# Optimization experiments

Measured on AMD Instinct MI355X. Metric: run time of the kernel, lower is better.

The kernel has to match this reference:

```python
import jax, jax.numpy as jnp
import numpy as np

EPS = 1e-5

def _lin(x, w, b):
    return x @ w + b

def _ln(x, scale, bias):
    m = jnp.mean(x, axis=-1, keepdims=True)
    v = jnp.var(x, axis=-1, keepdims=True)
    return (x - m) / jnp.sqrt(v + EPS) * scale + bias

def setup_inputs() -> dict:
    key = jax.random.key(0)
    B, N, F, OUT, TRI = 4, 128, 128, 128, 8
    ks = iter(jax.random.split(key, 64))
    def lin_params(fan_in, fan_out):
        s = 1.0 / np.sqrt(fan_in)
        w = jax.random.uniform(next(ks), (fan_in, fan_out), minval=-s, maxval=s, dtype=jnp.float32)
        b = jax.random.uniform(next(ks), (fan_out,), minval=-s, maxval=s, dtype=jnp.float32)
        return w, b
    inp = {}
    inp['node_fts'] = jax.random.normal(next(ks), (B, N, F), dtype=jnp.float32)
    inp['edge_fts'] = jax.random.normal(next(ks), (B, N, N, F), dtype=jnp.float32)
    inp['graph_fts'] = jax.random.normal(next(ks), (B, F), dtype=jnp.float32)
    inp['hidden'] = jax.random.normal(next(ks), (B, N, F), dtype=jnp.float32)
    inp['adj_matrix'] = jax.random.randint(next(ks), (B, N, N), 0, 2, dtype=jnp.int32)
    inp['m1_w'], inp['m1_b'] = lin_params(2 * F, OUT)
    inp['m2_w'], inp['m2_b'] = lin_params(2 * F, OUT)
    inp['me_w'], inp['me_b'] = lin_params(F, OUT)
    inp['mg_w'], inp['mg_b'] = lin_params(F, OUT)
    inp['mlp1_w'], inp['mlp1_b'] = lin_params(OUT, OUT)
    inp['mlp2_w'], inp['mlp2_b'] = lin_params(OUT, OUT)
    inp['o1_w'], inp['o1_b'] = lin_params(2 * F, OUT)
    inp['o2_w'], inp['o2_b'] = lin_params(OUT, OUT)
    inp['t1_w'], inp['t1_b'] = lin_params(2 * F, TRI)
    inp['t2_w'], inp['t2_b'] = lin_params(2 * F, TRI)
    inp['te1_w'], inp['te1_b'] = lin_params(F, TRI)
    inp['te2_w'], inp['te2_b'] = lin_params(F, TRI)
    inp['te3_w'], inp['te3_b'] = lin_params(F, TRI)
    inp['tg_w'], inp['tg_b'] = lin_params(F, TRI)
    inp['o3_w'], inp['o3_b'] = lin_params(TRI, OUT)
    inp['norm_scale'] = jnp.ones((OUT,), dtype=jnp.float32)
    inp['norm_bias'] = jnp.zeros((OUT,), dtype=jnp.float32)
    return inp

def reference(node_fts, edge_fts, graph_fts, hidden, adj_matrix,
              m1_w, m1_b, m2_w, m2_b, me_w, me_b, mg_w, mg_b,
              mlp1_w, mlp1_b, mlp2_w, mlp2_b,
              o1_w, o1_b, o2_w, o2_b,
              t1_w, t1_b, t2_w, t2_b,
              te1_w, te1_b, te2_w, te2_b, te3_w, te3_b,
              tg_w, tg_b, o3_w, o3_b, norm_scale, norm_bias):
    z = jnp.concatenate([node_fts, hidden], axis=-1)          # [B,N,2F]
    msg_1 = _lin(z, m1_w, m1_b)                                # [B,N,H]
    msg_2 = _lin(z, m2_w, m2_b)
    msg_e = _lin(edge_fts, me_w, me_b)                         # [B,N,N,H]
    msg_g = _lin(graph_fts, mg_w, mg_b)                        # [B,H]
    msgs = msg_1[:, None, :, :] + msg_2[:, :, None, :] + msg_e + msg_g[:, None, None, :]
    # msg_mlp: ReLU -> Linear -> ReLU -> Linear
    msgs = _lin(jax.nn.relu(_lin(jax.nn.relu(msgs), mlp1_w, mlp1_b)), mlp2_w, mlp2_b)
    # triplet messages (note: original code reuses t_1 for tri_3 -- faithful)
    tri_1 = _lin(z, t1_w, t1_b)                                # [B,N,T]
    tri_2 = _lin(z, t2_w, t2_b)
    tri_3 = _lin(z, t1_w, t1_b)
    tri_e_1 = _lin(edge_fts, te1_w, te1_b)                     # [B,N,N,T]
    tri_e_2 = _lin(edge_fts, te2_w, te2_b)
    tri_e_3 = _lin(edge_fts, te3_w, te3_b)
    tri_g = _lin(graph_fts, tg_w, tg_b)                        # [B,T]
    triplets = (tri_1[:, :, None, None, :] + tri_2[:, None, :, None, :]
                + tri_3[:, None, None, :, :]
                + tri_e_1[:, :, :, None, :] + tri_e_2[:, :, None, :, :]
                + tri_e_3[:, None, :, :, :]
                + tri_g[:, None, None, None, :])               # [B,N,N,N,T]
    tri_msgs = _lin(jnp.max(triplets, axis=1), o3_w, o3_b)     # [B,N,N,OUT]
    tri_msgs = _ln(jax.nn.relu(tri_msgs), norm_scale, norm_bias)
    # masked max aggregation
    maxarg = jnp.where(adj_matrix[..., None] == 1, msgs, -1e9)
    msgs_agg = jnp.max(maxarg, axis=1)                         # [B,N,H]
    out = jax.nn.relu(_lin(z, o1_w, o1_b) + _lin(msgs_agg, o2_w, o2_b))
    out = _ln(out, norm_scale, norm_bias)
    return out, tri_msgs
```

## Files before the change

kernel.cpp:

```cpp
#include <hip/hip_runtime.h>
#include <hip/hip_bf16.h>
#include <cstddef>
#include <cstdint>
#include <cstring>

typedef __attribute__((ext_vector_type(8))) short bf16x8;
typedef __attribute__((ext_vector_type(4))) float f32x4;
typedef unsigned short ushort_t;

__device__ __forceinline__ ushort_t f2b(float f) {
    uint32_t x = __float_as_uint(f);
    uint32_t r = (x + 0x7FFFu + ((x >> 16) & 1u)) >> 16;
    return (ushort_t)r;
}
__device__ __forceinline__ float b2f(ushort_t u) {
    return __uint_as_float(((uint32_t)u) << 16);
}
__device__ __forceinline__ uint32_t pk2(float x, float y) {
    __hip_bfloat162 h = __float22bfloat162_rn(float2{x, y});
    uint32_t u;
    __builtin_memcpy(&u, &h, 4);
    return u;
}

__global__ void prep_kernel(const float* __restrict__ m1_w, const float* __restrict__ m2_w,
                            const float* __restrict__ o1_w, const float* __restrict__ t1_w,
                            const float* __restrict__ t2_w,
                            const float* __restrict__ me_w, const float* __restrict__ mlp1_w,
                            const float* __restrict__ mlp2_w,
                            const float* __restrict__ te1_w, const float* __restrict__ te2_w,
                            const float* __restrict__ te3_w,
                            const float* __restrict__ graph_fts,
                            const float* __restrict__ mg_w, const float* __restrict__ mg_b,
                            const float* __restrict__ m1_b,
                            const float* __restrict__ tg_w, const float* __restrict__ t2_b,
                            const float* __restrict__ tg_b,
                            ushort_t* __restrict__ Wnt,
                            ushort_t* __restrict__ Wme, ushort_t* __restrict__ Wm1,
                            ushort_t* __restrict__ Wm2, ushort_t* __restrict__ TEt,
                            float* __restrict__ G1, float* __restrict__ TG) {
    int idx = blockIdx.x * 256 + threadIdx.x;
    if (idx < 106496) {
        int o = idx >> 8, k = idx & 255;
        float v = 0.0f;
        if (o < 128)       v = m1_w[k * 128 + o];
        else if (o < 256)  v = m2_w[k * 128 + (o - 128)];
        else if (o < 384)  v = o1_w[k * 128 + (o - 256)];
        else if (o < 392)  v = t1_w[k * 8 + (o - 384)];
        else if (o < 400)  v = t2_w[k * 8 + (o - 392)];
        Wnt[idx] = f2b(v);
    } else if (idx < 122880) {
        int t = idx - 106496, o = t >> 7, h = t & 127;
        Wme[t] = f2b(me_w[h * 128 + o]);
    } else if (idx < 139264) {
        int t = idx - 122880, o = t >> 7, h = t & 127;
        Wm1[t] = f2b(mlp1_w[h * 128 + o]);
    } else if (idx < 155648) {
        int t = idx - 139264, o = t >> 7, h = t & 127;
        Wm2[t] = f2b(mlp2_w[h * 128 + o]);
    } else if (idx < 159744) {
        int t = idx - 155648, c = t >> 7, h = t & 127;
        float v = 0.0f;
        if (c < 8)       v = te1_w[h * 8 + c];
        else if (c < 16) v = te2_w[h * 8 + (c - 8)];
        else if (c < 24) v = te3_w[h * 8 + (c - 16)];
        TEt[t] = f2b(v);
    } else if (idx < 160256) {
        int t = idx - 159744, b = t >> 7, h = t & 127;
        float a = m1_b[h] + mg_b[h];
        #pragma unroll 4
        for (int k = 0; k < 128; k++) a = fmaf(graph_fts[b * 128 + k], mg_w[k * 128 + h], a);
        G1[t] = a;
    } else if (idx < 160288) {
        int t = idx - 160256, b = t >> 3, tt = t & 7;
        float a = t2_b[tt] + tg_b[tt];
        #pragma unroll 4
        for (int k = 0; k < 128; k++) a = fmaf(graph_fts[b * 128 + k], tg_w[k * 8 + tt], a);
        TG[t] = a;
    }
}

__global__ __launch_bounds__(256)
void node_gemm(const float* __restrict__ node_fts, const float* __restrict__ hidden,
               const ushort_t* __restrict__ Wnt,
               const float* __restrict__ G1, const float* __restrict__ m2_b,
               const float* __restrict__ o1_b, const float* __restrict__ t1_b,
               const float* __restrict__ TG,
               float* __restrict__ M1, float* __restrict__ M2, float* __restrict__ O1z,
               float* __restrict__ T1v, float* __restrict__ TT2) {
    __shared__ ushort_t Zs[32 * 256];
    char* Zb = (char*)Zs;
    const int tid = threadIdx.x;
    const int blk = blockIdx.x;
    const int rowblk = blk >> 1, colh = blk & 1;
    const int b = rowblk >> 2, q = rowblk & 3;
    const int row0 = b * 128 + q * 32;
    const int w = tid >> 6, l = tid & 63, g = l >> 4, lq = l & 15;

    const float4* nsrc = reinterpret_cast<const float4*>(node_fts + (size_t)row0 * 128);
    const float4* hsrc = reinterpret_cast<const float4*>(hidden + (size_t)row0 * 128);
    #pragma unroll
    for (int p = 0; p < 8; p++) {
        int idx = tid + p * 256;
        int r = idx >> 6, c4 = idx & 63;
        float4 v = (c4 < 32) ? nsrc[r * 32 + c4] : hsrc[r * 32 + (c4 - 32)];
        uint2 pk;
        pk.x = pk2(v.x, v.y);
        pk.y = pk2(v.z, v.w);
        *reinterpret_cast<uint2*>(Zb + r * 512 + (((c4 >> 1) ^ (r & 7)) << 4) + (c4 & 1) * 8) = pk;
    }
    __syncthreads();

    for (int mt = colh * 13 + w; mt < colh * 13 + 13; mt += 4) {
        f32x4 acc0 = (f32x4){0.f, 0.f, 0.f, 0.f};
        f32x4 acc1 = (f32x4){0.f, 0.f, 0.f, 0.f};
        const ushort_t* arow = Wnt + (size_t)(mt * 16 + lq) * 256;
        #pragma unroll
        for (int ks = 0; ks < 8; ks++) {
            bf16x8 a = *reinterpret_cast<const bf16x8*>(arow + ks * 32 + g * 8);
            int j0 = lq, j1 = 16 + lq;
            bf16x8 b0 = *reinterpret_cast<const bf16x8*>(Zb + j0 * 512 + (((ks * 4 + g) ^ (j0 & 7)) << 4));
            bf16x8 b1 = *reinterpret_cast<const bf16x8*>(Zb + j1 * 512 + (((ks * 4 + g) ^ (j1 & 7)) << 4));
            acc0 = __builtin_amdgcn_mfma_f32_16x16x32_bf16(a, b0, acc0, 0, 0, 0);
            acc1 = __builtin_amdgcn_mfma_f32_16x16x32_bf16(a, b1, acc1, 0, 0, 0);
        }
        #pragma unroll
        for (int half = 0; half < 2; half++) {
            const f32x4 acc = half ? acc1 : acc0;
            const int grow = row0 + half * 16 + lq;
            #pragma unroll
            for (int c = 0; c < 4; c++) {
                int o = mt * 16 + g * 4 + c;
                float v = acc[c];
                if (o < 128)       M1[(size_t)grow * 128 + o] = v + G1[b * 128 + o];
                else if (o < 256)  M2[(size_t)grow * 128 + (o - 128)] = v + m2_b[o - 128];
                else if (o < 384)  O1z[(size_t)grow * 128 + (o - 256)] = v + o1_b[o - 256];
                else if (o < 392)  T1v[(size_t)grow * 8 + (o - 384)] = v + t1_b[o - 384];
                else if (o < 400)  TT2[(size_t)grow * 8 + (o - 392)] = v + TG[b * 8 + (o - 392)];
            }
        }
    }
}

__device__ __forceinline__ void mmv(const ushort_t* __restrict__ Wt, const char* Xa,
                                    f32x4 acc[2][4], int o_blk, int j_blk, int g, int lq) {
    #pragma unroll
    for (int ks = 0; ks < 4; ks++) {
        bf16x8 a[2], bb[4];
        #pragma unroll
        for (int m = 0; m < 2; m++)
            a[m] = *reinterpret_cast<const bf16x8*>(Wt + (size_t)(o_blk + m * 16 + lq) * 128 + ks * 32 + g * 8);
        #pragma unroll
        for (int n = 0; n < 4; n++) {
            int j = j_blk + n * 16 + lq;
            bb[n] = *reinterpret_cast<const bf16x8*>(Xa + j * 256 + (((ks * 4 + g) ^ (j & 7)) << 4));
        }
        #pragma unroll
        for (int m = 0; m < 2; m++)
            #pragma unroll
            for (int n = 0; n < 4; n++)
                acc[m][n] = __builtin_amdgcn_mfma_f32_16x16x32_bf16(a[m], bb[n], acc[m][n], 0, 0, 0);
    }
}

__global__ __launch_bounds__(512, 4)
void edge_kernel(const float* __restrict__ edge_fts,
                 const ushort_t* __restrict__ Wme, const float* __restrict__ me_b,
                 const ushort_t* __restrict__ Wm1, const float* __restrict__ mlp1_b,
                 const ushort_t* __restrict__ Wm2, const float* __restrict__ mlp2_b,
                 const ushort_t* __restrict__ TEt,
                 const float* __restrict__ te1_b, const float* __restrict__ te2_b,
                 const float* __restrict__ te3_b,
                 const float* __restrict__ M1,  const float* __restrict__ M2,
                 const float* __restrict__ T1v, const float* __restrict__ TT2,
                 const int* __restrict__ adj, const float* __restrict__ O1z,
                 const float* __restrict__ o2_w, const float* __restrict__ o2_b,
                 const float* __restrict__ nsc, const float* __restrict__ nbi,
                 float* __restrict__ out,
                 float* __restrict__ T1buf, float* __restrict__ T2buf,
                 float* __restrict__ E3buf) {
    __shared__ ushort_t Xs[2][16384];
    char* X0 = (char*)Xs[0];
    char* X1 = (char*)Xs[1];
    const int tid = threadIdx.x;
    const int b  = blockIdx.x >> 7;
    const int jf = blockIdx.x & 127;
    const int w = tid >> 6, l = tid & 63, g = l >> 4, lq = l & 15;
    const int o_blk = (w & 3) * 32, j_blk = (w >> 2) * 64;

    #pragma unroll
    for (int p = 0; p < 8; p++) {
        int idx = tid + p * 512;
        int r = idx >> 5, c4 = idx & 31;
        const float4* src = reinterpret_cast<const float4*>(
            edge_fts + ((size_t)(b * 128 + r) * 128 + jf) * 128);
        float4 v = src[c4];
        uint2 pk;
        pk.x = pk2(v.x, v.y);
        pk.y = pk2(v.z, v.w);
        *reinterpret_cast<uint2*>(X0 + r * 256 + (((c4 >> 1) ^ (r & 7)) << 4) + (c4 & 1) * 8) = pk;
    }
    __syncthreads();

    {
        const int m_te = w & 1;
        const int jq = (w >> 1) & 3;
        const ushort_t* At = TEt + m_te * 16 * 128;
        f32x4 acc2[2];
        #pragma unroll
        for (int n = 0; n < 2; n++) acc2[n] = (f32x4){0.f, 0.f, 0.f, 0.f};
        #pragma unroll
        for (int ks = 0; ks < 4; ks++) {
            bf16x8 a = *reinterpret_cast<const bf16x8*>(At + lq * 128 + ks * 32 + g * 8);
            #pragma unroll
            for (int n = 0; n < 2; n++) {
                int j = jq * 32 + n * 16 + lq;
                bf16x8 bbv = *reinterpret_cast<const bf16x8*>(X0 + j * 256 + (((ks * 4 + g) ^ (j & 7)) << 4));
                acc2[n] = __builtin_amdgcn_mfma_f32_16x16x32_bf16(a, bbv, acc2[n], 0, 0, 0);
            }
        }
        if (m_te == 0) {
            if (g < 2) {
                int t0 = g * 4;
                const float4 eb = *reinterpret_cast<const float4*>(te1_b + t0);
                #pragma unroll
                for (int n = 0; n < 2; n++) {
                    int r = jq * 32 + n * 16 + lq;
                    const float4 tv = *reinterpret_cast<const float4*>(T1v + (size_t)(b * 128 + r) * 8 + t0);
                    float4 o4 = make_float4(acc2[n][0] + eb.x + tv.x, acc2[n][1] + eb.y + tv.y,
                                            acc2[n][2] + eb.z + tv.z, acc2[n][3] + eb.w + tv.w);
                    *reinterpret_cast<float4*>(T1buf + ((size_t)(b * 128 + jf) * 128 + r) * 8 + t0) = o4;
                }
            } else {
                int t0 = g * 4 - 8;
                const float4 eb = *reinterpret_cast<const float4*>(te2_b + t0);
                #pragma unroll
                for (int n = 0; n < 2; n++) {
                    int r = jq * 32 + n * 16 + lq;
                    float4 o4 = make_float4(acc2[n][0] + eb.x, acc2[n][1] + eb.y,
                                            acc2[n][2] + eb.z, acc2[n][3] + eb.w);
                    *reinterpret_cast<float4*>(T2buf + ((size_t)(b * 128 + r) * 128 + jf) * 8 + t0) = o4;
                }
            }
        } else if (g < 2) {
            int t0 = g * 4;
            const float4 eb = *reinterpret_cast<const float4*>(te3_b + t0);
            const float4 t3v = *reinterpret_cast<const float4*>(T1v + (size_t)(b * 128 + jf) * 8 + t0);
            #pragma unroll
            for (int n = 0; n < 2; n++) {
                int r = jq * 32 + n * 16 + lq;
                const float4 t2v = *reinterpret_cast<const float4*>(TT2 + (size_t)(b * 128 + r) * 8 + t0);
                float4 o4 = make_float4(acc2[n][0] + eb.x + t2v.x + t3v.x,
                                        acc2[n][1] + eb.y + t2v.y + t3v.y,
                                        acc2[n][2] + eb.z + t2v.z + t3v.z,
                                        acc2[n][3] + eb.w + t2v.w + t3v.w);
                *reinterpret_cast<float4*>(E3buf + ((size_t)(b * 128 + r) * 128 + jf) * 8 + t0) = o4;
            }
        }
    }

    f32x4 acc[2][4];

    #pragma unroll
    for (int m = 0; m < 2; m++)
        #pragma unroll
        for (int n = 0; n < 4; n++) acc[m][n] = (f32x4){0.f, 0.f, 0.f, 0.f};
    mmv(Wme, X0, acc, o_blk, j_blk, g, lq);
    {
        #pragma unroll
        for (int m = 0; m < 2; m++) {
            int o0 = o_blk + m * 16 + g * 4;
            const float4 eb = *reinterpret_cast<const float4*>(me_b + o0);
            const float4 m1 = *reinterpret_cast<const float4*>(M1 + (size_t)(b * 128 + jf) * 128 + o0);
            float4 bc = make_float4(eb.x + m1.x, eb.y + m1.y, eb.z + m1.z, eb.w + m1.w);
            #pragma unroll
            for (int n = 0; n < 4; n++) {
                int j = j_blk + n * 16 + lq;
                const float4 m2 = *reinterpret_cast<const float4*>(M2 + (size_t)(b * 128 + j) * 128 + o0);
                float r0 = fmaxf(acc[m][n][0] + bc.x + m2.x, 0.f);
                float r1 = fmaxf(acc[m][n][1] + bc.y + m2.y, 0.f);
                float r2 = fmaxf(acc[m][n][2] + bc.z + m2.z, 0.f);
                float r3 = fmaxf(acc[m][n][3] + bc.w + m2.w, 0.f);
                uint2 pk;
                pk.x = pk2(r0, r1);
                pk.y = pk2(r2, r3);
                *reinterpret_cast<uint2*>(X1 + j * 256 + ((((o0 >> 3) ^ (j & 7))) << 4) + (o0 & 7) * 2) = pk;
            }
        }
        __syncthreads();
    }

    #pragma unroll
    for (int m = 0; m < 2; m++)
        #pragma unroll
        for (int n = 0; n < 4; n++) acc[m][n] = (f32x4){0.f, 0.f, 0.f, 0.f};
    mmv(Wm1, X1, acc, o_blk, j_blk, g, lq);
    {
        #pragma unroll
        for (int m = 0; m < 2; m++) {
            int o0 = o_blk + m * 16 + g * 4;
            const float4 bb = *reinterpret_cast<const float4*>(mlp1_b + o0);
            #pragma unroll
            for (int n = 0; n < 4; n++) {
                int j = j_blk + n * 16 + lq;
                float r0 = fmaxf(acc[m][n][0] + bb.x, 0.f);
                float r1 = fmaxf(acc[m][n][1] + bb.y, 0.f);
                float r2 = fmaxf(acc[m][n][2] + bb.z, 0.f);
                float r3 = fmaxf(acc[m][n][3] + bb.w, 0.f);
                uint2 pk;
                pk.x = pk2(r0, r1);
                pk.y = pk2(r2, r3);
                *reinterpret_cast<uint2*>(X0 + j * 256 + ((((o0 >> 3) ^ (j & 7))) << 4) + (o0 & 7) * 2) = pk;
            }
        }
        __syncthreads();
    }

    #pragma unroll
    for (int m = 0; m < 2; m++)
        #pragma unroll
        for (int n = 0; n < 4; n++) acc[m][n] = (f32x4){0.f, 0.f, 0.f, 0.f};
    mmv(Wm2, X0, acc, o_blk, j_blk, g, lq);
    {
        #pragma unroll
        for (int m = 0; m < 2; m++) {
            int o0 = o_blk + m * 16 + g * 4;
            const float4 bb = *reinterpret_cast<const float4*>(mlp2_b + o0);
            #pragma unroll
            for (int n = 0; n < 4; n++) {
                int j = j_blk + n * 16 + lq;
                float r0 = acc[m][n][0] + bb.x;
                float r1 = acc[m][n][1] + bb.y;
                float r2 = acc[m][n][2] + bb.z;
                float r3 = acc[m][n][3] + bb.w;
                uint2 pk;
                pk.x = pk2(r0, r1);
                pk.y = pk2(r2, r3);
                *reinterpret_cast<uint2*>(X1 + j * 256 + ((((o0 >> 3) ^ (j & 7))) << 4) + (o0 & 7) * 2) = pk;
            }
        }
        __syncthreads();
    }

    {
        float* scr  = reinterpret_cast<float*>(X0);
        float* aggs = scr;
        float* fagg = scr + 512;
        float* sums = scr + 640;
        float* red  = scr + 1152;
        const int h = tid & 127, wv = tid >> 7;
        {
            const int* acol = adj + b * 16384 + jf;
            float amax = -1e9f;
            #pragma unroll 8
            for (int s = 0; s < 32; s++) {
                int r = wv * 32 + s;
                ushort_t u = *reinterpret_cast<const ushort_t*>(
                    X1 + r * 256 + (((h >> 3) ^ (r & 7)) << 4) + (h & 7) * 2);
                amax = (acol[r * 128] == 1) ? fmaxf(amax, b2f(u)) : amax;
            }
            aggs[wv * 128 + h] = amax;
        }
        __syncthreads();
        if (tid < 128)
            fagg[tid] = fmaxf(fmaxf(aggs[tid], aggs[128 + tid]),
                              fmaxf(aggs[256 + tid], aggs[384 + tid]));
        __syncthreads();
        {
            float part = 0.f;
            const float* wcol = o2_w + h;
            #pragma unroll 8
            for (int k = wv * 32; k < wv * 32 + 32; k++)
                part = fmaf(fagg[k], wcol[k * 128], part);
            sums[wv * 128 + h] = part;
        }
        __syncthreads();
        float v = 0.f;
        if (tid < 128) {
            float val = o2_b[h] + O1z[(size_t)(b * 128 + jf) * 128 + h]
                      + sums[h] + sums[128 + h] + sums[256 + h] + sums[384 + h];
            v = fmaxf(val, 0.f);
        }
        float s = v, s2 = v * v;
        #pragma unroll
        for (int off = 32; off >= 1; off >>= 1) {
            s  += __shfl_down(s, off, 64);
            s2 += __shfl_down(s2, off, 64);
        }
        if (tid < 128 && (tid & 63) == 0) { red[tid >> 6] = s; red[2 + (tid >> 6)] = s2; }
        __syncthreads();
        if (tid < 128) {
            const float tot = red[0] + red[1], tot2 = red[2] + red[3];
            const float mean = tot * (1.0f / 128.0f);
            const float var = tot2 * (1.0f / 128.0f) - mean * mean;
            const float rstd = rsqrtf(var + 1e-5f);
            out[(size_t)(b * 128 + jf) * 128 + h] = (v - mean) * rstd * nsc[h] + nbi[h];
        }
    }
}

__global__ __launch_bounds__(512)
void tri_kernel(const float* __restrict__ T1buf, const float* __restrict__ T2buf,
                const float* __restrict__ E3buf, const float* __restrict__ o3_w,
                const float* __restrict__ o3_b, const float* __restrict__ scale,
                const float* __restrict__ bias, float* __restrict__ tri_out) {
    __shared__ __align__(16) float T1s[1024];
    __shared__ __align__(16) float E3s[1024];
    __shared__ __align__(16) float o3s[1024];
    __shared__ __align__(16) float Ps[4][128][8];
    const int b = blockIdx.x >> 7, jf = blockIdx.x & 127;
    const int tid = threadIdx.x;
    if (tid < 256) {
        reinterpret_cast<float4*>(T1s)[tid] =
            reinterpret_cast<const float4*>(T1buf + (size_t)(b * 128 + jf) * 1024)[tid];
        reinterpret_cast<float4*>(o3s)[tid] = reinterpret_cast<const float4*>(o3_w)[tid];
    } else {
        int t2 = tid - 256;
        reinterpret_cast<float4*>(E3s)[t2] =
            reinterpret_cast<const float4*>(E3buf + (size_t)(b * 128 + jf) * 1024)[t2];
    }
    __syncthreads();

    {
        const int kf = tid & 127, ih = tid >> 7;
        float a8[8];
        #pragma unroll
        for (int t = 0; t < 8; t++) a8[t] = -3.0e38f;
        const float4* t2p = reinterpret_cast<const float4*>(T2buf + (size_t)b * 131072);
        #pragma unroll 4
        for (int ii = 0; ii < 32; ++ii) {
            const int i = ih * 32 + ii;
            const float4 p = t2p[(i * 128 + kf) * 2];
            const float4 q = t2p[(i * 128 + kf) * 2 + 1];
            const float* t1r = &T1s[i * 8];
            a8[0] = fmaxf(a8[0], t1r[0] + p.x);
            a8[1] = fmaxf(a8[1], t1r[1] + p.y);
            a8[2] = fmaxf(a8[2], t1r[2] + p.z);
            a8[3] = fmaxf(a8[3], t1r[3] + p.w);
            a8[4] = fmaxf(a8[4], t1r[4] + q.x);
            a8[5] = fmaxf(a8[5], t1r[5] + q.y);
            a8[6] = fmaxf(a8[6], t1r[6] + q.z);
            a8[7] = fmaxf(a8[7], t1r[7] + q.w);
        }
        #pragma unroll
        for (int t = 0; t < 8; t++) Ps[ih][kf][t] = a8[t];
    }
    __syncthreads();

    const int w = tid >> 6, l = tid & 63;
    const float ob0 = o3_b[l],     ob1 = o3_b[l + 64];
    const float sc0 = scale[l],    sc1 = scale[l + 64];
    const float bi0 = bias[l],     bi1 = bias[l + 64];
    for (int kk = 0; kk < 16; ++kk) {
        const int kf = w * 16 + kk;
        float m8[8];
        #pragma unroll
        for (int t = 0; t < 8; t++)
            m8[t] = fmaxf(fmaxf(Ps[0][kf][t], Ps[1][kf][t]),
                          fmaxf(Ps[2][kf][t], Ps[3][kf][t])) + E3s[kf * 8 + t];
        float v0 = ob0, v1 = ob1;
        #pragma unroll
        for (int t = 0; t < 8; t++) {
            v0 = fmaf(m8[t], o3s[t * 128 + l], v0);
            v1 = fmaf(m8[t], o3s[t * 128 + l + 64], v1);
        }
        v0 = fmaxf(v0, 0.0f);
        v1 = fmaxf(v1, 0.0f);
        float s = v0 + v1, s2 = v0 * v0 + v1 * v1;
        #pragma unroll
        for (int off = 32; off >= 1; off >>= 1) {
            s  += __shfl_xor(s, off, 64);
            s2 += __shfl_xor(s2, off, 64);
        }
        const float mean = s * (1.0f / 128.0f);
        const float var = s2 * (1.0f / 128.0f) - mean * mean;
        const float rstd = rsqrtf(var + 1e-5f);
        float* dst = tri_out + (size_t)((b * 128 + jf) * 128 + kf) * 128;
        dst[l]      = (v0 - mean) * rstd * sc0 + bi0;
        dst[l + 64] = (v1 - mean) * rstd * sc1 + bi1;
    }
}

extern "C" void kernel_launch(void* const* d_in, const int* in_sizes, int n_in,
                              void* d_out, int out_size, void* d_ws, size_t ws_size,
                              hipStream_t stream) {
    const float* node_fts  = (const float*)d_in[0];
    const float* edge_fts  = (const float*)d_in[1];
    const float* graph_fts = (const float*)d_in[2];
    const float* hidden    = (const float*)d_in[3];
    const int*   adj       = (const int*)d_in[4];
    const float* m1_w = (const float*)d_in[5],  *m1_b = (const float*)d_in[6];
    const float* m2_w = (const float*)d_in[7],  *m2_b = (const float*)d_in[8];
    const float* me_w = (const float*)d_in[9],  *me_b = (const float*)d_in[10];
    const float* mg_w = (const float*)d_in[11], *mg_b = (const float*)d_in[12];
    const float* mlp1_w = (const float*)d_in[13], *mlp1_b = (const float*)d_in[14];
    const float* mlp2_w = (const float*)d_in[15], *mlp2_b = (const float*)d_in[16];
    const float* o1_w = (const float*)d_in[17], *o1_b = (const float*)d_in[18];
    const float* o2_w = (const float*)d_in[19], *o2_b = (const float*)d_in[20];
    const float* t1_w = (const float*)d_in[21], *t1_b = (const float*)d_in[22];
    const float* t2_w = (const float*)d_in[23], *t2_b = (const float*)d_in[24];
    const float* te1_w = (const float*)d_in[25], *te1_b = (const float*)d_in[26];
    const float* te2_w = (const float*)d_in[27], *te2_b = (const float*)d_in[28];
    const float* te3_w = (const float*)d_in[29], *te3_b = (const float*)d_in[30];
    const float* tg_w = (const float*)d_in[31], *tg_b = (const float*)d_in[32];
    const float* o3_w = (const float*)d_in[33], *o3_b = (const float*)d_in[34];
    const float* norm_scale = (const float*)d_in[35];
    const float* norm_bias  = (const float*)d_in[36];

    char* w8 = (char*)d_ws;
    float*    M1    = (float*)(w8 + 0);
    float*    M2    = (float*)(w8 + 262144);
    float*    O1z   = (float*)(w8 + 524288);
    float*    T1v   = (float*)(w8 + 786432);
    float*    TT2   = (float*)(w8 + 802816);
    ushort_t* Wme   = (ushort_t*)(w8 + 819200);
    ushort_t* Wm1   = (ushort_t*)(w8 + 851968);
    ushort_t* Wm2   = (ushort_t*)(w8 + 884736);
    ushort_t* TEt   = (ushort_t*)(w8 + 917504);
    float*    T1buf = (float*)(w8 + 17702912);
    float*    T2buf = (float*)(w8 + 19800064);
    float*    E3buf = (float*)(w8 + 21897216);
    ushort_t* Wnt   = (ushort_t*)(w8 + 23994368);
    float*    G1    = (float*)(w8 + 24207360);
    float*    TG    = (float*)(w8 + 24209408);

    float* out_p  = (float*)d_out;
    float* tri_p  = (float*)d_out + 65536;

    prep_kernel<<<627, 256, 0, stream>>>(m1_w, m2_w, o1_w, t1_w, t2_w,
                                         me_w, mlp1_w, mlp2_w, te1_w, te2_w, te3_w,
                                         graph_fts, mg_w, mg_b, m1_b, tg_w, t2_b, tg_b,
                                         Wnt, Wme, Wm1, Wm2, TEt, G1, TG);
    node_gemm<<<32, 256, 0, stream>>>(node_fts, hidden, Wnt, G1, m2_b, o1_b, t1_b, TG,
                                      M1, M2, O1z, T1v, TT2);
    edge_kernel<<<512, 512, 0, stream>>>(edge_fts, Wme, me_b, Wm1, mlp1_b, Wm2, mlp2_b,
                                         TEt, te1_b, te2_b, te3_b,
                                         M1, M2, T1v, TT2,
                                         adj, O1z, o2_w, o2_b, norm_scale, norm_bias,
                                         out_p, T1buf, T2buf, E3buf);
    tri_kernel<<<512, 512, 0, stream>>>(T1buf, T2buf, E3buf, o3_w, o3_b,
                                        norm_scale, norm_bias, tri_p);
}
```

Measured before the change: 93.99 us.

## Store triplet intermediate buffers in bf16 and simplify node LayerNorm epilogue

The T1/T2/E3 triplet intermediates written by the edge kernel and read by the tri kernel are now packed as bf16 instead of fp32. This halves their global write and read traffic, including the heavily reread T2 buffer in the tri max loop, at the cost of reduced precision in the triplet sums. Separately, the node-output LayerNorm is now done by a single wave that handles two features per lane. That removes a shared-memory reduction and a block barrier, and its parameter loads are hoisted earlier.

```diff
diff --git a/kernel.cpp b/kernel.cpp
--- a/kernel.cpp
+++ b/kernel.cpp
@@ -177,8 +177,8 @@
                  const float* __restrict__ o2_w, const float* __restrict__ o2_b,
                  const float* __restrict__ nsc, const float* __restrict__ nbi,
                  float* __restrict__ out,
-                 float* __restrict__ T1buf, float* __restrict__ T2buf,
-                 float* __restrict__ E3buf) {
+                 ushort_t* __restrict__ T1buf, ushort_t* __restrict__ T2buf,
+                 ushort_t* __restrict__ E3buf) {
     __shared__ ushort_t Xs[2][16384];
     char* X0 = (char*)Xs[0];
     char* X1 = (char*)Xs[1];
@@ -227,9 +227,10 @@
                 for (int n = 0; n < 2; n++) {
                     int r = jq * 32 + n * 16 + lq;
                     const float4 tv = *reinterpret_cast<const float4*>(T1v + (size_t)(b * 128 + r) * 8 + t0);
-                    float4 o4 = make_float4(acc2[n][0] + eb.x + tv.x, acc2[n][1] + eb.y + tv.y,
-                                            acc2[n][2] + eb.z + tv.z, acc2[n][3] + eb.w + tv.w);
-                    *reinterpret_cast<float4*>(T1buf + ((size_t)(b * 128 + jf) * 128 + r) * 8 + t0) = o4;
+                    uint2 pkv;
+                    pkv.x = pk2(acc2[n][0] + eb.x + tv.x, acc2[n][1] + eb.y + tv.y);
+                    pkv.y = pk2(acc2[n][2] + eb.z + tv.z, acc2[n][3] + eb.w + tv.w);
+                    *reinterpret_cast<uint2*>(T1buf + ((size_t)(b * 128 + jf) * 128 + r) * 8 + t0) = pkv;
                 }
             } else {
                 int t0 = g * 4 - 8;
@@ -237,9 +238,10 @@
                 #pragma unroll
                 for (int n = 0; n < 2; n++) {
                     int r = jq * 32 + n * 16 + lq;
-                    float4 o4 = make_float4(acc2[n][0] + eb.x, acc2[n][1] + eb.y,
-                                            acc2[n][2] + eb.z, acc2[n][3] + eb.w);
-                    *reinterpret_cast<float4*>(T2buf + ((size_t)(b * 128 + r) * 128 + jf) * 8 + t0) = o4;
+                    uint2 pkv;
+                    pkv.x = pk2(acc2[n][0] + eb.x, acc2[n][1] + eb.y);
+                    pkv.y = pk2(acc2[n][2] + eb.z, acc2[n][3] + eb.w);
+                    *reinterpret_cast<uint2*>(T2buf + ((size_t)(b * 128 + r) * 128 + jf) * 8 + t0) = pkv;
                 }
             }
         } else if (g < 2) {
@@ -250,11 +252,10 @@
             for (int n = 0; n < 2; n++) {
                 int r = jq * 32 + n * 16 + lq;
                 const float4 t2v = *reinterpret_cast<const float4*>(TT2 + (size_t)(b * 128 + r) * 8 + t0);
-                float4 o4 = make_float4(acc2[n][0] + eb.x + t2v.x + t3v.x,
-                                        acc2[n][1] + eb.y + t2v.y + t3v.y,
-                                        acc2[n][2] + eb.z + t2v.z + t3v.z,
-                                        acc2[n][3] + eb.w + t2v.w + t3v.w);
-                *reinterpret_cast<float4*>(E3buf + ((size_t)(b * 128 + r) * 128 + jf) * 8 + t0) = o4;
+                uint2 pkv;
+                pkv.x = pk2(acc2[n][0] + eb.x + t2v.x + t3v.x, acc2[n][1] + eb.y + t2v.y + t3v.y);
+                pkv.y = pk2(acc2[n][2] + eb.z + t2v.z + t3v.z, acc2[n][3] + eb.w + t2v.w + t3v.w);
+                *reinterpret_cast<uint2*>(E3buf + ((size_t)(b * 128 + r) * 128 + jf) * 8 + t0) = pkv;
             }
         }
     }
@@ -347,8 +348,16 @@
         float* aggs = scr;
         float* fagg = scr + 512;
         float* sums = scr + 640;
-        float* red  = scr + 1152;
         const int h = tid & 127, wv = tid >> 7;
+        float o1zv0 = 0.f, o1zv1 = 0.f, ob0 = 0.f, ob1 = 0.f;
+        float sc0 = 0.f, sc1 = 0.f, bi0 = 0.f, bi1 = 0.f;
+        if (w == 0) {
+            const float* o1p = O1z + (size_t)(b * 128 + jf) * 128;
+            o1zv0 = o1p[l];      o1zv1 = o1p[l + 64];
+            ob0 = o2_b[l];       ob1 = o2_b[l + 64];
+            sc0 = nsc[l];        sc1 = nsc[l + 64];
+            bi0 = nbi[l];        bi1 = nbi[l + 64];
+        }
         {
             const int* acol = adj + b * 16384 + jf;
             float amax = -1e9f;
@@ -375,33 +384,28 @@
             sums[wv * 128 + h] = part;
         }
         __syncthreads();
-        float v = 0.f;
-        if (tid < 128) {
-            float val = o2_b[h] + O1z[(size_t)(b * 128 + jf) * 128 + h]
-                      + sums[h] + sums[128 + h] + sums[256 + h] + sums[384 + h];
-            v = fmaxf(val, 0.f);
-        }
-        float s = v, s2 = v * v;
-        #pragma unroll
-        for (int off = 32; off >= 1; off >>= 1) {
-            s  += __shfl_down(s, off, 64);
-            s2 += __shfl_down(s2, off, 64);
-        }
-        if (tid < 128 && (tid & 63) == 0) { red[tid >> 6] = s; red[2 + (tid >> 6)] = s2; }
-        __syncthreads();
-        if (tid < 128) {
-            const float tot = red[0] + red[1], tot2 = red[2] + red[3];
-            const float mean = tot * (1.0f / 128.0f);
-            const float var = tot2 * (1.0f / 128.0f) - mean * mean;
+        if (w == 0) {
+            float v0 = fmaxf(ob0 + o1zv0 + sums[l] + sums[128 + l] + sums[256 + l] + sums[384 + l], 0.f);
+            float v1 = fmaxf(ob1 + o1zv1 + sums[l + 64] + sums[128 + l + 64] + sums[256 + l + 64] + sums[384 + l + 64], 0.f);
+            float s = v0 + v1, s2 = v0 * v0 + v1 * v1;
+            #pragma unroll
+            for (int off = 32; off >= 1; off >>= 1) {
+                s  += __shfl_xor(s, off, 64);
+                s2 += __shfl_xor(s2, off, 64);
+            }
+            const float mean = s * (1.0f / 128.0f);
+            const float var = s2 * (1.0f / 128.0f) - mean * mean;
             const float rstd = rsqrtf(var + 1e-5f);
-            out[(size_t)(b * 128 + jf) * 128 + h] = (v - mean) * rstd * nsc[h] + nbi[h];
+            float* dst = out + (size_t)(b * 128 + jf) * 128;
+            dst[l]      = (v0 - mean) * rstd * sc0 + bi0;
+            dst[l + 64] = (v1 - mean) * rstd * sc1 + bi1;
         }
     }
 }
 
 __global__ __launch_bounds__(512)
-void tri_kernel(const float* __restrict__ T1buf, const float* __restrict__ T2buf,
-                const float* __restrict__ E3buf, const float* __restrict__ o3_w,
+void tri_kernel(const ushort_t* __restrict__ T1buf, const ushort_t* __restrict__ T2buf,
+                const ushort_t* __restrict__ E3buf, const float* __restrict__ o3_w,
                 const float* __restrict__ o3_b, const float* __restrict__ scale,
                 const float* __restrict__ bias, float* __restrict__ tri_out) {
     __shared__ __align__(16) float T1s[1024];
@@ -410,14 +414,24 @@
     __shared__ __align__(16) float Ps[4][128][8];
     const int b = blockIdx.x >> 7, jf = blockIdx.x & 127;
     const int tid = threadIdx.x;
-    if (tid < 256) {
-        reinterpret_cast<float4*>(T1s)[tid] =
-            reinterpret_cast<const float4*>(T1buf + (size_t)(b * 128 + jf) * 1024)[tid];
-        reinterpret_cast<float4*>(o3s)[tid] = reinterpret_cast<const float4*>(o3_w)[tid];
+    if (tid < 128) {
+        uint4 u = reinterpret_cast<const uint4*>(T1buf + (size_t)(b * 128 + jf) * 1024)[tid];
+        float* d = &T1s[tid * 8];
+        d[0] = b2f((ushort_t)u.x); d[1] = b2f((ushort_t)(u.x >> 16));
+        d[2] = b2f((ushort_t)u.y); d[3] = b2f((ushort_t)(u.y >> 16));
+        d[4] = b2f((ushort_t)u.z); d[5] = b2f((ushort_t)(u.z >> 16));
+        d[6] = b2f((ushort_t)u.w); d[7] = b2f((ushort_t)(u.w >> 16));
+    } else if (tid < 256) {
+        int t = tid - 128;
+        uint4 u = reinterpret_cast<const uint4*>(E3buf + (size_t)(b * 128 + jf) * 1024)[t];
+        float* d = &E3s[t * 8];
+        d[0] = b2f((ushort_t)u.x); d[1] = b2f((ushort_t)(u.x >> 16));
+        d[2] = b2f((ushort_t)u.y); d[3] = b2f((ushort_t)(u.y >> 16));
+        d[4] = b2f((ushort_t)u.z); d[5] = b2f((ushort_t)(u.z >> 16));
+        d[6] = b2f((ushort_t)u.w); d[7] = b2f((ushort_t)(u.w >> 16));
     } else {
-        int t2 = tid - 256;
-        reinterpret_cast<float4*>(E3s)[t2] =
-            reinterpret_cast<const float4*>(E3buf + (size_t)(b * 128 + jf) * 1024)[t2];
+        int t = tid - 256;
+        reinterpret_cast<float4*>(o3s)[t] = reinterpret_cast<const float4*>(o3_w)[t];
     }
     __syncthreads();
 
@@ -426,21 +440,20 @@
         float a8[8];
         #pragma unroll
         for (int t = 0; t < 8; t++) a8[t] = -3.0e38f;
-        const float4* t2p = reinterpret_cast<const float4*>(T2buf + (size_t)b * 131072);
+        const uint4* t2p = reinterpret_cast<const uint4*>(T2buf + (size_t)b * 131072);
         #pragma unroll 4
         for (int ii = 0; ii < 32; ++ii) {
             const int i = ih * 32 + ii;
-            const float4 p = t2p[(i * 128 + kf) * 2];
-            const float4 q = t2p[(i * 128 + kf) * 2 + 1];
+            uint4 u = t2p[i * 128 + kf];
             const float* t1r = &T1s[i * 8];
-            a8[0] = fmaxf(a8[0], t1r[0] + p.x);
-            a8[1] = fmaxf(a8[1], t1r[1] + p.y);
-            a8[2] = fmaxf(a8[2], t1r[2] + p.z);
-            a8[3] = fmaxf(a8[3], t1r[3] + p.w);
-            a8[4] = fmaxf(a8[4], t1r[4] + q.x);
-            a8[5] = fmaxf(a8[5], t1r[5] + q.y);
-            a8[6] = fmaxf(a8[6], t1r[6] + q.z);
-            a8[7] = fmaxf(a8[7], t1r[7] + q.w);
+            a8[0] = fmaxf(a8[0], t1r[0] + b2f((ushort_t)u.x));
+            a8[1] = fmaxf(a8[1], t1r[1] + b2f((ushort_t)(u.x >> 16)));
+            a8[2] = fmaxf(a8[2], t1r[2] + b2f((ushort_t)u.y));
+            a8[3] = fmaxf(a8[3], t1r[3] + b2f((ushort_t)(u.y >> 16)));
+            a8[4] = fmaxf(a8[4], t1r[4] + b2f((ushort_t)u.z));
+            a8[5] = fmaxf(a8[5], t1r[5] + b2f((ushort_t)(u.z >> 16)));
+            a8[6] = fmaxf(a8[6], t1r[6] + b2f((ushort_t)u.w));
+            a8[7] = fmaxf(a8[7], t1r[7] + b2f((ushort_t)(u.w >> 16)));
         }
         #pragma unroll
         for (int t = 0; t < 8; t++) Ps[ih][kf][t] = a8[t];
@@ -517,9 +530,9 @@
     ushort_t* Wm1   = (ushort_t*)(w8 + 851968);
     ushort_t* Wm2   = (ushort_t*)(w8 + 884736);
     ushort_t* TEt   = (ushort_t*)(w8 + 917504);
-    float*    T1buf = (float*)(w8 + 17702912);
-    float*    T2buf = (float*)(w8 + 19800064);
-    float*    E3buf = (float*)(w8 + 21897216);
+    ushort_t* T1buf = (ushort_t*)(w8 + 17702912);
+    ushort_t* T2buf = (ushort_t*)(w8 + 19800064);
+    ushort_t* E3buf = (ushort_t*)(w8 + 21897216);
     ushort_t* Wnt   = (ushort_t*)(w8 + 23994368);
     float*    G1    = (float*)(w8 + 24207360);
     float*    TG    = (float*)(w8 + 24209408);
```

After: 89.76 us (median of 2 runs). -4.5%, faster.
